# Kernel optimization log

Measured on AMD Instinct MI355X. Metric: run time of the kernel, lower is better.

Reference implementation:

```python
import jax, jax.numpy as jnp
import numpy as np

N, D = 8192, 4096


def setup_inputs() -> dict:
    key = jax.random.key(0)
    k1, k2, k3 = jax.random.split(key, 3)
    x = jax.random.normal(k1, (N, D), jnp.float32)
    W = jax.random.normal(k2, (D, D), jnp.float32) / np.sqrt(D)  # nn.Linear weight [out,in]
    b = jax.random.normal(k3, (D,), jnp.float32) * 0.01
    recency_weight = jnp.full((1,), -0.1, jnp.float32)
    return {"x": x, "W": W, "b": b, "recency_weight": recency_weight}


def reference(x, W, b, recency_weight):
    # linear -> relu projection
    x_proj = jax.nn.relu(x @ W.T + b)  # [N, D]
    # self-similarity
    scores = x_proj @ x_proj.T  # [N, N]
    n = scores.shape[0]
    idx = jnp.arange(n)
    # triu mask with diagonal=0 (use_current_timestep=False): keep strictly lower triangle
    mask = idx[None, :] >= idx[:, None]
    scores = jnp.where(mask, -jnp.inf, scores)
    # recency bias: toeplitz(arange(n)) == |i - j|, zeroed on masked positions
    rec = jnp.abs(idx[:, None] - idx[None, :]).astype(scores.dtype)
    rec = jnp.where(mask, 0.0, rec)
    scores = scores + recency_weight[0] * rec
    # row 0 is fully masked (-inf everywhere); replace with finite values to avoid
    # NaN in softmax -- the row is overwritten with zeros afterwards anyway.
    scores = scores.at[0].set(0.0)
    attn = jax.nn.softmax(scores, axis=1)
    attn = attn.at[0].set(0.0)  # matches scores[0] = zeros in the torch code
    return attn
```

## Files before the change

### kernel.cpp

```cpp
#include <hip/hip_runtime.h>
#include <hip/hip_bf16.h>
#include <stdint.h>

typedef _Float16 f16_t;
typedef f16_t f16x8_t __attribute__((ext_vector_type(8)));
typedef f16_t f16x4_t __attribute__((ext_vector_type(4)));
typedef float f32x4_t __attribute__((ext_vector_type(4)));

#define NROWS 8192
#define DDIM  4096
#define BK 32
#define KTILES (DDIM / BK)
#define LSTR 40

__device__ __forceinline__ void gload16(const void* g, void* s) {
  __builtin_amdgcn_global_load_lds(
      (const __attribute__((address_space(1))) void*)g,
      (__attribute__((address_space(3))) void*)s, 16, 0, 0);
}

__global__ __launch_bounds__(256) void k_split(const float* __restrict__ in,
                                               f16_t* __restrict__ hi,
                                               f16_t* __restrict__ lo) {
  const long i = ((long)blockIdx.x * 256 + threadIdx.x) * 4;
  const float4 v = *reinterpret_cast<const float4*>(in + i);
  float vv[4] = {v.x, v.y, v.z, v.w};
  f16x4_t h, l;
#pragma unroll
  for (int c = 0; c < 4; ++c) {
    f16_t hh = (f16_t)vv[c];
    h[c] = hh;
    l[c] = (f16_t)(vv[c] - (float)hh);
  }
  *reinterpret_cast<f16x4_t*>(hi + i) = h;
  *reinterpret_cast<f16x4_t*>(lo + i) = l;
}

typedef f16_t lds4_t[4][256][BK];

__device__ __forceinline__ void gemm_core256_g1(
    const f16_t* __restrict__ pAh, const f16_t* __restrict__ pAl, long lda,
    const f16_t* __restrict__ pBh, const f16_t* __restrict__ pBl, long ldb,
    lds4_t* sm, f32x4_t (&acc)[8][4]) {
  const int t = threadIdx.x, lane = t & 63, w = t >> 6;
  const int fr = lane & 15, kg = lane >> 4;
  const int wr = (w >> 2) * 128, wc = (w & 3) * 64;
  const int w32 = w * 32;
  const int sr0 = w32 + (lane >> 2);
  const int sg = (((lane & 3) ^ ((lane >> 3) & 3)) * 8);
  const int kge = (kg ^ ((fr >> 1) & 3)) * 8;

#pragma unroll
  for (int m = 0; m < 8; ++m)
#pragma unroll
    for (int n = 0; n < 4; ++n) acc[m][n] = f32x4_t{0.f, 0.f, 0.f, 0.f};

  const f16_t* gAh = pAh + (long)sr0 * lda + sg;
  const f16_t* gAl = pAl + (long)sr0 * lda + sg;
  const f16_t* gBh = pBh + (long)sr0 * ldb + sg;
  const f16_t* gBl = pBl + (long)sr0 * ldb + sg;
  const long a16 = 16 * lda, b16 = 16 * ldb;

  auto issue = [&](int buf, int plane, const f16_t* g, long ld16, int k0) {
    gload16(g + k0, &sm[buf][plane][w32][0]);
    gload16(g + ld16 + k0, &sm[buf][plane][w32 + 16][0]);
  };

  f16x8_t ah[8], al[8], bh[4], bl[4];
  auto read8 = [&](f16x8_t(&R)[8], int buf, int plane) {
#pragma unroll
    for (int m = 0; m < 8; ++m)
      R[m] = *reinterpret_cast<const f16x8_t*>(&sm[buf][plane][wr + m * 16 + fr][kge]);
  };
  auto read4 = [&](f16x8_t(&R)[4], int buf, int plane) {
#pragma unroll
    for (int n = 0; n < 4; ++n)
      R[n] = *reinterpret_cast<const f16x8_t*>(&sm[buf][plane][wc + n * 16 + fr][kge]);
  };
  auto mfma32 = [&](f16x8_t(&A)[8], f16x8_t(&B)[4]) {
    __builtin_amdgcn_s_setprio(1);
#pragma unroll
    for (int m = 0; m < 8; ++m)
#pragma unroll
      for (int n = 0; n < 4; ++n)
        acc[m][n] = __builtin_amdgcn_mfma_f32_16x16x32_f16(A[m], B[n], acc[m][n], 0, 0, 0);
    __builtin_amdgcn_s_setprio(0);
  };

  issue(0, 0, gAh, a16, 0);
  issue(0, 2, gBh, b16, 0);
  issue(0, 3, gBl, b16, 0);
  issue(0, 1, gAl, a16, 0);
  asm volatile("s_waitcnt vmcnt(0)" ::: "memory");
  __builtin_amdgcn_s_barrier();

  for (int kt = 0; kt < KTILES - 1; ++kt) {
    const int c = kt & 1;
    const int k0 = (kt + 1) * BK;
    issue(c ^ 1, 0, gAh, a16, k0);
    issue(c ^ 1, 2, gBh, b16, k0);
    issue(c ^ 1, 3, gBl, b16, k0);
    read8(ah, c, 0);
    read4(bh, c, 2);
    read4(bl, c, 3);
    asm volatile("s_waitcnt lgkmcnt(0)" ::: "memory");
    mfma32(ah, bh);
    mfma32(ah, bl);
    asm volatile("s_waitcnt vmcnt(6)" ::: "memory");
    __builtin_amdgcn_s_barrier();
    read8(al, c, 1);
    issue(c ^ 1, 1, gAl, a16, k0);
    asm volatile("s_waitcnt lgkmcnt(0)" ::: "memory");
    mfma32(al, bh);
    asm volatile("s_waitcnt vmcnt(2)" ::: "memory");
    __builtin_amdgcn_s_barrier();
  }
  {
    const int c = (KTILES - 1) & 1;
    read8(ah, c, 0);
    read4(bh, c, 2);
    read4(bl, c, 3);
    asm volatile("s_waitcnt lgkmcnt(0)" ::: "memory");
    mfma32(ah, bh);
    mfma32(ah, bl);
    asm volatile("s_waitcnt vmcnt(0)" ::: "memory");
    __builtin_amdgcn_s_barrier();
    read8(al, c, 1);
    asm volatile("s_waitcnt lgkmcnt(0)" ::: "memory");
    mfma32(al, bh);
  }
}

typedef f16_t lds3_t[3][256][BK];

__device__ __forceinline__ void gemm_core256_g2(
    const f16_t* __restrict__ pAh, long lda,
    const f16_t* __restrict__ pBh, const f16_t* __restrict__ pBl, long ldb,
    lds3_t* sm, f32x4_t (&acc)[8][4], bool diag) {
  const int t = threadIdx.x, lane = t & 63, w = t >> 6;
  const int fr = lane & 15, kg = lane >> 4;
  const int wr = (w >> 2) * 128, wc = (w & 3) * 64;
  const int w32 = w * 32;
  const int sr0 = w32 + (lane >> 2);
  const int sg = (((lane & 3) ^ ((lane >> 3) & 3)) * 8);
  const int kge = (kg ^ ((fr >> 1) & 3)) * 8;
  const bool skipw = diag && (wr == 0) && (wc >= 128);

#pragma unroll
  for (int m = 0; m < 8; ++m)
#pragma unroll
    for (int n = 0; n < 4; ++n) acc[m][n] = f32x4_t{0.f, 0.f, 0.f, 0.f};

  const f16_t* gAh = pAh + (long)sr0 * lda + sg;
  const f16_t* gBh = pBh + (long)sr0 * ldb + sg;
  const f16_t* gBl = pBl + (long)sr0 * ldb + sg;
  const long a16 = 16 * lda, b16 = 16 * ldb;

  auto issue = [&](int buf, int plane, const f16_t* g, long ld16, int k0) {
    gload16(g + k0, &sm[buf][plane][w32][0]);
    gload16(g + ld16 + k0, &sm[buf][plane][w32 + 16][0]);
  };

  f16x8_t ah[8], bh[4], bl[4];
  auto read8 = [&](f16x8_t(&R)[8], int buf, int plane) {
#pragma unroll
    for (int m = 0; m < 8; ++m)
      R[m] = *reinterpret_cast<const f16x8_t*>(&sm[buf][plane][wr + m * 16 + fr][kge]);
  };
  auto read4 = [&](f16x8_t(&R)[4], int buf, int plane) {
#pragma unroll
    for (int n = 0; n < 4; ++n)
      R[n] = *reinterpret_cast<const f16x8_t*>(&sm[buf][plane][wc + n * 16 + fr][kge]);
  };
  auto mfma32 = [&](f16x8_t(&A)[8], f16x8_t(&B)[4]) {
    __builtin_amdgcn_s_setprio(1);
#pragma unroll
    for (int m = 0; m < 8; ++m)
#pragma unroll
      for (int n = 0; n < 4; ++n)
        acc[m][n] = __builtin_amdgcn_mfma_f32_16x16x32_f16(A[m], B[n], acc[m][n], 0, 0, 0);
    __builtin_amdgcn_s_setprio(0);
  };

  issue(0, 0, gAh, a16, 0);
  issue(0, 1, gBh, b16, 0);
  issue(0, 2, gBl, b16, 0);
  asm volatile("s_waitcnt vmcnt(0)" ::: "memory");
  __builtin_amdgcn_s_barrier();

  for (int kt = 0; kt < KTILES - 1; ++kt) {
    const int c = kt & 1;
    const int k0 = (kt + 1) * BK;
    issue(c ^ 1, 0, gAh, a16, k0);
    issue(c ^ 1, 1, gBh, b16, k0);
    if (!skipw) {
      read8(ah, c, 0);
      read4(bh, c, 1);
      asm volatile("s_waitcnt lgkmcnt(0)" ::: "memory");
      mfma32(ah, bh);
    }
    asm volatile("s_waitcnt vmcnt(4)" ::: "memory");
    __builtin_amdgcn_s_barrier();
    if (!skipw) {
      read4(bl, c, 2);
    }
    issue(c ^ 1, 2, gBl, b16, k0);
    if (!skipw) {
      asm volatile("s_waitcnt lgkmcnt(0)" ::: "memory");
      mfma32(ah, bl);
    }
    asm volatile("s_waitcnt vmcnt(2)" ::: "memory");
    __builtin_amdgcn_s_barrier();
  }
  {
    const int c = (KTILES - 1) & 1;
    if (!skipw) {
      read8(ah, c, 0);
      read4(bh, c, 1);
      asm volatile("s_waitcnt lgkmcnt(0)" ::: "memory");
      mfma32(ah, bh);
    }
    asm volatile("s_waitcnt vmcnt(0)" ::: "memory");
    __builtin_amdgcn_s_barrier();
    if (!skipw) {
      read4(bl, c, 2);
      asm volatile("s_waitcnt lgkmcnt(0)" ::: "memory");
      mfma32(ah, bl);
    }
  }
}

__global__ __launch_bounds__(512, 2) void k_gemm1_256(
    const f16_t* __restrict__ xh, const f16_t* __restrict__ xl,
    const f16_t* __restrict__ Wh, const f16_t* __restrict__ Wl,
    const float* __restrict__ bias,
    f16_t* __restrict__ xph, f16_t* __restrict__ xpl) {
  extern __shared__ char smraw[];
  lds4_t* sm = (lds4_t*)smraw;

  int bid = (int)blockIdx.x;
  bid = (bid & 7) * 64 + (bid >> 3);
  const int bx = bid & 15, by = bid >> 4;
  const long brow = (long)by * 256, bcol = (long)bx * 256;

  f32x4_t acc[8][4];
  gemm_core256_g1(xh + brow * DDIM, xl + brow * DDIM, DDIM,
                  Wh + bcol * DDIM, Wl + bcol * DDIM, DDIM, sm, acc);

  const int t = threadIdx.x, lane = t & 63, w = t >> 6;
  const int wr = (w >> 2) * 128, wc = (w & 3) * 64;
  const int cr = (lane >> 4) * 4, cc = lane & 15;
#pragma unroll
  for (int n = 0; n < 4; ++n) {
    const long col = bcol + wc + n * 16 + cc;
    const float bb = bias[col];
#pragma unroll
    for (int m = 0; m < 8; ++m) {
      const long row0 = brow + wr + m * 16 + cr;
#pragma unroll
      for (int r = 0; r < 4; ++r) {
        const float v = fmaxf(acc[m][n][r] + bb, 0.f);
        const f16_t h = (f16_t)v;
        xph[(row0 + r) * (long)DDIM + col] = h;
        xpl[(row0 + r) * (long)DDIM + col] = (f16_t)(v - (float)h);
      }
    }
  }
}

__global__ __launch_bounds__(512, 2) void k_gemm2_256(
    const f16_t* __restrict__ xph, const f16_t* __restrict__ xpl,
    const float* __restrict__ rwp, float* __restrict__ out) {
  extern __shared__ char smraw[];
  lds3_t* sm = (lds3_t*)smraw;

  int bid = (int)blockIdx.x;
  bid = (bid & 7) * 66 + (bid >> 3);
  int by = (int)((sqrtf(8.f * (float)bid + 1.f) - 1.f) * 0.5f);
  while ((by + 1) * (by + 2) / 2 <= bid) ++by;
  while (by * (by + 1) / 2 > bid) --by;
  const int bx = bid - by * (by + 1) / 2;

  const long brow = (long)by * 256, bcol = (long)bx * 256;
  f32x4_t acc[8][4];
  gemm_core256_g2(xph + brow * DDIM, DDIM,
                  xph + bcol * DDIM, xpl + bcol * DDIM, DDIM, sm, acc, bx == by);

  const float rw = rwp[0];
  const int t = threadIdx.x, lane = t & 63, w = t >> 6;
  const int wr = (w >> 2) * 128, wc = (w & 3) * 64;
  const int cr = (lane >> 4) * 4, cc = lane & 15;
#pragma unroll
  for (int n = 0; n < 4; ++n) {
    const long gj = bcol + wc + n * 16 + cc;
#pragma unroll
    for (int m = 0; m < 8; ++m) {
      const long gi0 = brow + wr + m * 16 + cr;
#pragma unroll
      for (int r = 0; r < 4; ++r) {
        const long gi = gi0 + r;
        out[gi * (long)NROWS + gj] = acc[m][n][r] + rw * (float)(gi - gj);
      }
    }
  }
}

__device__ __forceinline__ void stage_split(const float* __restrict__ src, long ld,
                                            f16_t (&hi)[128][LSTR],
                                            f16_t (&lo)[128][LSTR],
                                            int t) {
#pragma unroll
  for (int i = 0; i < 4; ++i) {
    const int f = i * 256 + t;
    const int row = f >> 3;
    const int kq = (f & 7) << 2;
    const float4 v = *reinterpret_cast<const float4*>(src + (long)row * ld + kq);
    float vv[4] = {v.x, v.y, v.z, v.w};
    f16x4_t h, l;
#pragma unroll
    for (int c = 0; c < 4; ++c) {
      f16_t hh = (f16_t)vv[c];
      h[c] = hh;
      l[c] = (f16_t)(vv[c] - (float)hh);
    }
    *reinterpret_cast<f16x4_t*>(&hi[row][kq]) = h;
    *reinterpret_cast<f16x4_t*>(&lo[row][kq]) = l;
  }
}

__global__ __launch_bounds__(256) void k_gemm1_slow(
    const float* __restrict__ x, const float* __restrict__ W,
    const float* __restrict__ bias,
    f16_t* __restrict__ xph, f16_t* __restrict__ xpl) {
  __shared__ alignas(16) f16_t Ahi[128][LSTR];
  __shared__ alignas(16) f16_t Alo[128][LSTR];
  __shared__ alignas(16) f16_t Bhi[128][LSTR];
  __shared__ alignas(16) f16_t Blo[128][LSTR];

  const long brow = (long)blockIdx.y * 128;
  const long bcol = (long)blockIdx.x * 128;
  const int t = threadIdx.x, lane = t & 63;
  const int wr = ((t >> 6) >> 1) * 64, wc = ((t >> 6) & 1) * 64;
  const int fr = lane & 15, kg = lane >> 4;

  f32x4_t acc[4][4];
#pragma unroll
  for (int m = 0; m < 4; ++m)
#pragma unroll
    for (int n = 0; n < 4; ++n) acc[m][n] = f32x4_t{0.f, 0.f, 0.f, 0.f};

  const float* Abase = x + brow * DDIM;
  const float* Bbase = W + bcol * DDIM;
  for (int k0 = 0; k0 < DDIM; k0 += BK) {
    __syncthreads();
    stage_split(Abase + k0, DDIM, Ahi, Alo, t);
    stage_split(Bbase + k0, DDIM, Bhi, Blo, t);
    __syncthreads();

    f16x8_t ah[4], al[4], bh[4], bl[4];
#pragma unroll
    for (int m = 0; m < 4; ++m) {
      ah[m] = *reinterpret_cast<const f16x8_t*>(&Ahi[wr + m * 16 + fr][kg * 8]);
      al[m] = *reinterpret_cast<const f16x8_t*>(&Alo[wr + m * 16 + fr][kg * 8]);
      bh[m] = *reinterpret_cast<const f16x8_t*>(&Bhi[wc + m * 16 + fr][kg * 8]);
      bl[m] = *reinterpret_cast<const f16x8_t*>(&Blo[wc + m * 16 + fr][kg * 8]);
    }
#pragma unroll
    for (int m = 0; m < 4; ++m)
#pragma unroll
      for (int n = 0; n < 4; ++n) {
        acc[m][n] = __builtin_amdgcn_mfma_f32_16x16x32_f16(ah[m], bh[n], acc[m][n], 0, 0, 0);
        acc[m][n] = __builtin_amdgcn_mfma_f32_16x16x32_f16(ah[m], bl[n], acc[m][n], 0, 0, 0);
        acc[m][n] = __builtin_amdgcn_mfma_f32_16x16x32_f16(al[m], bh[n], acc[m][n], 0, 0, 0);
      }
  }

  const int cr = (lane >> 4) * 4, cc = lane & 15;
#pragma unroll
  for (int n = 0; n < 4; ++n) {
    const long col = bcol + wc + n * 16 + cc;
    const float bb = bias[col];
#pragma unroll
    for (int m = 0; m < 4; ++m) {
      const long row0 = brow + wr + m * 16 + cr;
#pragma unroll
      for (int r = 0; r < 4; ++r) {
        const float v = fmaxf(acc[m][n][r] + bb, 0.f);
        const f16_t h = (f16_t)v;
        xph[(row0 + r) * (long)DDIM + col] = h;
        xpl[(row0 + r) * (long)DDIM + col] = (f16_t)(v - (float)h);
      }
    }
  }
}

__global__ __launch_bounds__(256) void k_row_softmax(float* __restrict__ out, int n) {
  const int i = blockIdx.x;
  float* row = out + (size_t)i * n;
  const int L = i;
  const int t = threadIdx.x;
  __shared__ float redm[4], reds[4];

  float m = -3.0e38f, s = 0.f;
  for (int j = t; j < L; j += 256) {
    const float v = row[j];
    const float M = fmaxf(m, v);
    s = s * __expf(m - M) + __expf(v - M);
    m = M;
  }
#pragma unroll
  for (int o = 32; o > 0; o >>= 1) {
    const float om = __shfl_down(m, o, 64);
    const float os = __shfl_down(s, o, 64);
    const float M = fmaxf(m, om);
    s = s * __expf(m - M) + os * __expf(om - M);
    m = M;
  }
  if ((t & 63) == 0) { redm[t >> 6] = m; reds[t >> 6] = s; }
  __syncthreads();
  const float M4 = fmaxf(fmaxf(redm[0], redm[1]), fmaxf(redm[2], redm[3]));
  const float S4 = reds[0] * __expf(redm[0] - M4) + reds[1] * __expf(redm[1] - M4) +
                   reds[2] * __expf(redm[2] - M4) + reds[3] * __expf(redm[3] - M4);
  const float inv = (L > 0) ? 1.f / S4 : 0.f;

  for (int j = t; j < n; j += 256) {
    row[j] = (j < L) ? __expf(row[j] - M4) * inv : 0.f;
  }
}

extern "C" void kernel_launch(void* const* d_in, const int* in_sizes, int n_in,
                              void* d_out, int out_size, void* d_ws, size_t ws_size,
                              hipStream_t stream) {
  (void)in_sizes; (void)n_in; (void)out_size;
  const float* x = (const float*)d_in[0];
  const float* W = (const float*)d_in[1];
  const float* b = (const float*)d_in[2];
  const float* rw = (const float*)d_in[3];
  float* out = (float*)d_out;

  const size_t NX = (size_t)NROWS * DDIM;
  const size_t NW = (size_t)DDIM * DDIM;
  char* ws = (char*)d_ws;
  f16_t* xph = (f16_t*)ws;
  f16_t* xpl = (f16_t*)(ws + NX * 2);

  const int LDSB1 = 2 * 4 * 256 * BK * 2;
  const int LDSB2 = 2 * 3 * 256 * BK * 2;
  (void)hipFuncSetAttribute(reinterpret_cast<const void*>(k_gemm1_256),
                            hipFuncAttributeMaxDynamicSharedMemorySize, LDSB1);
  (void)hipFuncSetAttribute(reinterpret_cast<const void*>(k_gemm2_256),
                            hipFuncAttributeMaxDynamicSharedMemorySize, LDSB2);

  const size_t need_full = NX * 4  + NX * 4  + NW * 4 ;
  if (ws_size >= need_full) {
    f16_t* xh = (f16_t*)(ws + NX * 4);
    f16_t* xl = (f16_t*)(ws + NX * 6);
    f16_t* Wh = (f16_t*)(ws + NX * 8);
    f16_t* Wl = (f16_t*)(ws + NX * 8 + NW * 2);
    k_split<<<(int)(NX / 1024), 256, 0, stream>>>(x, xh, xl);
    k_split<<<(int)(NW / 1024), 256, 0, stream>>>(W, Wh, Wl);
    k_gemm1_256<<<512, 512, LDSB1, stream>>>(xh, xl, Wh, Wl, b, xph, xpl);
  } else {
    k_gemm1_slow<<<dim3(DDIM / 128, NROWS / 128), 256, 0, stream>>>(x, W, b, xph, xpl);
  }

  const int ntri = (NROWS / 256) * (NROWS / 256 + 1) / 2;
  k_gemm2_256<<<ntri, 512, LDSB2, stream>>>(xph, xpl, rw, out);
  k_row_softmax<<<NROWS, 256, 0, stream>>>(out, NROWS);
}
```

Before: 1.422 ms.

## Pack diagonal tiles two per block and drop explicit LDS waits before MFMA

The second GEMM grid goes from 528 triangular tiles to exactly 512 blocks. The first 16 blocks each process two half-work diagonal tiles in sequence, and the remaining 496 blocks each take one strictly-lower off-diagonal tile through a new index mapping. With two blocks per CU this is meant to fit the launch into a single wave and remove the small tail of leftover blocks. Separately, the explicit lgkmcnt(0) waits before the MFMA groups are removed in both GEMM cores, leaving the compiler to insert the finer-grained waits it needs so LDS reads can overlap with math. The risk is that the compiler's waits turn out no better than before, and the paired diagonal blocks become a longer critical path.

Result: faster. 1.387 ms (-2.5%).

```diff
diff --git a/kernel.cpp b/kernel.cpp
--- a/kernel.cpp
+++ b/kernel.cpp
@@ -103,14 +103,12 @@
     read8(ah, c, 0);
     read4(bh, c, 2);
     read4(bl, c, 3);
-    asm volatile("s_waitcnt lgkmcnt(0)" ::: "memory");
     mfma32(ah, bh);
     mfma32(ah, bl);
     asm volatile("s_waitcnt vmcnt(6)" ::: "memory");
     __builtin_amdgcn_s_barrier();
     read8(al, c, 1);
     issue(c ^ 1, 1, gAl, a16, k0);
-    asm volatile("s_waitcnt lgkmcnt(0)" ::: "memory");
     mfma32(al, bh);
     asm volatile("s_waitcnt vmcnt(2)" ::: "memory");
     __builtin_amdgcn_s_barrier();
@@ -120,13 +118,11 @@
     read8(ah, c, 0);
     read4(bh, c, 2);
     read4(bl, c, 3);
-    asm volatile("s_waitcnt lgkmcnt(0)" ::: "memory");
     mfma32(ah, bh);
     mfma32(ah, bl);
     asm volatile("s_waitcnt vmcnt(0)" ::: "memory");
     __builtin_amdgcn_s_barrier();
     read8(al, c, 1);
-    asm volatile("s_waitcnt lgkmcnt(0)" ::: "memory");
     mfma32(al, bh);
   }
 }
@@ -196,7 +192,6 @@
     if (!skipw) {
       read8(ah, c, 0);
       read4(bh, c, 1);
-      asm volatile("s_waitcnt lgkmcnt(0)" ::: "memory");
       mfma32(ah, bh);
     }
     asm volatile("s_waitcnt vmcnt(4)" ::: "memory");
@@ -206,7 +201,6 @@
     }
     issue(c ^ 1, 2, gBl, b16, k0);
     if (!skipw) {
-      asm volatile("s_waitcnt lgkmcnt(0)" ::: "memory");
       mfma32(ah, bl);
     }
     asm volatile("s_waitcnt vmcnt(2)" ::: "memory");
@@ -217,14 +211,12 @@
     if (!skipw) {
       read8(ah, c, 0);
       read4(bh, c, 1);
-      asm volatile("s_waitcnt lgkmcnt(0)" ::: "memory");
       mfma32(ah, bh);
     }
     asm volatile("s_waitcnt vmcnt(0)" ::: "memory");
     __builtin_amdgcn_s_barrier();
     if (!skipw) {
       read4(bl, c, 2);
-      asm volatile("s_waitcnt lgkmcnt(0)" ::: "memory");
       mfma32(ah, bl);
     }
   }
@@ -268,40 +260,56 @@
   }
 }
 
+__device__ __forceinline__ void g2_epilogue(f32x4_t (&acc)[8][4], long brow, long bcol,
+                                            float rw, float* __restrict__ out) {
+  const int t = threadIdx.x, lane = t & 63, w = t >> 6;
+  const int wr = (w >> 2) * 128, wc = (w & 3) * 64;
+  const int cr = (lane >> 4) * 4, cc = lane & 15;
+#pragma unroll
+  for (int n = 0; n < 4; ++n) {
+    const long gj = bcol + wc + n * 16 + cc;
+#pragma unroll
+    for (int m = 0; m < 8; ++m) {
+      const long gi0 = brow + wr + m * 16 + cr;
+#pragma unroll
+      for (int r = 0; r < 4; ++r) {
+        const long gi = gi0 + r;
+        out[gi * (long)NROWS + gj] = acc[m][n][r] + rw * (float)(gi - gj);
+      }
+    }
+  }
+}
+
 __global__ __launch_bounds__(512, 2) void k_gemm2_256(
     const f16_t* __restrict__ xph, const f16_t* __restrict__ xpl,
     const float* __restrict__ rwp, float* __restrict__ out) {
   extern __shared__ char smraw[];
   lds3_t* sm = (lds3_t*)smraw;
-
-  int bid = (int)blockIdx.x;
-  bid = (bid & 7) * 66 + (bid >> 3);
-  int by = (int)((sqrtf(8.f * (float)bid + 1.f) - 1.f) * 0.5f);
-  while ((by + 1) * (by + 2) / 2 <= bid) ++by;
-  while (by * (by + 1) / 2 > bid) --by;
-  const int bx = bid - by * (by + 1) / 2;
-
-  const long brow = (long)by * 256, bcol = (long)bx * 256;
+  const float rw = rwp[0];
+  const int bid = (int)blockIdx.x;
+
   f32x4_t acc[8][4];
-  gemm_core256_g2(xph + brow * DDIM, DDIM,
-                  xph + bcol * DDIM, xpl + bcol * DDIM, DDIM, sm, acc, bx == by);
-
-  const float rw = rwp[0];
-  const int t = threadIdx.x, lane = t & 63, w = t >> 6;
-  const int wr = (w >> 2) * 128, wc = (w & 3) * 64;
-  const int cr = (lane >> 4) * 4, cc = lane & 15;
-#pragma unroll
-  for (int n = 0; n < 4; ++n) {
-    const long gj = bcol + wc + n * 16 + cc;
-#pragma unroll
-    for (int m = 0; m < 8; ++m) {
-      const long gi0 = brow + wr + m * 16 + cr;
-#pragma unroll
-      for (int r = 0; r < 4; ++r) {
-        const long gi = gi0 + r;
-        out[gi * (long)NROWS + gj] = acc[m][n][r] + rw * (float)(gi - gj);
-      }
-    }
+  if (bid < 16) {
+#pragma unroll 1
+    for (int d = 0; d < 2; ++d) {
+      const int by = bid * 2 + d;
+      const long brow = (long)by * 256, bcol = brow;
+      gemm_core256_g2(xph + brow * DDIM, DDIM,
+                      xph + bcol * DDIM, xpl + bcol * DDIM, DDIM, sm, acc, true);
+      g2_epilogue(acc, brow, bcol, rw, out);
+      __syncthreads();
+    }
+  } else {
+    int p = bid - 16;
+    p = (p & 7) * 62 + (p >> 3);
+    int by = (int)((1.f + sqrtf(1.f + 8.f * (float)p)) * 0.5f);
+    while (by * (by + 1) / 2 <= p) ++by;
+    while (by * (by - 1) / 2 > p) --by;
+    const int bx = p - by * (by - 1) / 2;
+    const long brow = (long)by * 256, bcol = (long)bx * 256;
+    gemm_core256_g2(xph + brow * DDIM, DDIM,
+                    xph + bcol * DDIM, xpl + bcol * DDIM, DDIM, sm, acc, false);
+    g2_epilogue(acc, brow, bcol, rw, out);
   }
 }
 
@@ -464,7 +472,6 @@
     k_gemm1_slow<<<dim3(DDIM / 128, NROWS / 128), 256, 0, stream>>>(x, W, b, xph, xpl);
   }
 
-  const int ntri = (NROWS / 256) * (NROWS / 256 + 1) / 2;
-  k_gemm2_256<<<ntri, 512, LDSB2, stream>>>(xph, xpl, rw, out);
+  k_gemm2_256<<<512, 512, LDSB2, stream>>>(xph, xpl, rw, out);
   k_row_softmax<<<NROWS, 256, 0, stream>>>(out, NROWS);
 }
```

## Retile second GEMM to 128x256 triangular tiles with higher occupancy

Applied to the files above, without the earlier changes.

Replaces the 256x256 triangular-tile self-similarity GEMM with a 128x256 tile kernel that uses a single packed LDS buffer and smaller accumulators, allowing four blocks per CU. The finer row granularity cuts wasted work on diagonal tiles and rebalances the triangular grid. It also removes the explicit lgkmcnt waits before the MFMAs in the first GEMM, leaving LDS read ordering to the compiler. The trade-off is less operand reuse per tile and more global traffic, plus a risk that the compiler's implicit waits will not cover the removed ones.

New measurement: 1.734 ms. +22.0%, slower.

```diff
diff --git a/kernel.cpp b/kernel.cpp
--- a/kernel.cpp
+++ b/kernel.cpp
@@ -103,14 +103,12 @@
     read8(ah, c, 0);
     read4(bh, c, 2);
     read4(bl, c, 3);
-    asm volatile("s_waitcnt lgkmcnt(0)" ::: "memory");
     mfma32(ah, bh);
     mfma32(ah, bl);
     asm volatile("s_waitcnt vmcnt(6)" ::: "memory");
     __builtin_amdgcn_s_barrier();
     read8(al, c, 1);
     issue(c ^ 1, 1, gAl, a16, k0);
-    asm volatile("s_waitcnt lgkmcnt(0)" ::: "memory");
     mfma32(al, bh);
     asm volatile("s_waitcnt vmcnt(2)" ::: "memory");
     __builtin_amdgcn_s_barrier();
@@ -120,113 +118,12 @@
     read8(ah, c, 0);
     read4(bh, c, 2);
     read4(bl, c, 3);
-    asm volatile("s_waitcnt lgkmcnt(0)" ::: "memory");
     mfma32(ah, bh);
     mfma32(ah, bl);
     asm volatile("s_waitcnt vmcnt(0)" ::: "memory");
     __builtin_amdgcn_s_barrier();
     read8(al, c, 1);
-    asm volatile("s_waitcnt lgkmcnt(0)" ::: "memory");
     mfma32(al, bh);
-  }
-}
-
-typedef f16_t lds3_t[3][256][BK];
-
-__device__ __forceinline__ void gemm_core256_g2(
-    const f16_t* __restrict__ pAh, long lda,
-    const f16_t* __restrict__ pBh, const f16_t* __restrict__ pBl, long ldb,
-    lds3_t* sm, f32x4_t (&acc)[8][4], bool diag) {
-  const int t = threadIdx.x, lane = t & 63, w = t >> 6;
-  const int fr = lane & 15, kg = lane >> 4;
-  const int wr = (w >> 2) * 128, wc = (w & 3) * 64;
-  const int w32 = w * 32;
-  const int sr0 = w32 + (lane >> 2);
-  const int sg = (((lane & 3) ^ ((lane >> 3) & 3)) * 8);
-  const int kge = (kg ^ ((fr >> 1) & 3)) * 8;
-  const bool skipw = diag && (wr == 0) && (wc >= 128);
-
-#pragma unroll
-  for (int m = 0; m < 8; ++m)
-#pragma unroll
-    for (int n = 0; n < 4; ++n) acc[m][n] = f32x4_t{0.f, 0.f, 0.f, 0.f};
-
-  const f16_t* gAh = pAh + (long)sr0 * lda + sg;
-  const f16_t* gBh = pBh + (long)sr0 * ldb + sg;
-  const f16_t* gBl = pBl + (long)sr0 * ldb + sg;
-  const long a16 = 16 * lda, b16 = 16 * ldb;
-
-  auto issue = [&](int buf, int plane, const f16_t* g, long ld16, int k0) {
-    gload16(g + k0, &sm[buf][plane][w32][0]);
-    gload16(g + ld16 + k0, &sm[buf][plane][w32 + 16][0]);
-  };
-
-  f16x8_t ah[8], bh[4], bl[4];
-  auto read8 = [&](f16x8_t(&R)[8], int buf, int plane) {
-#pragma unroll
-    for (int m = 0; m < 8; ++m)
-      R[m] = *reinterpret_cast<const f16x8_t*>(&sm[buf][plane][wr + m * 16 + fr][kge]);
-  };
-  auto read4 = [&](f16x8_t(&R)[4], int buf, int plane) {
-#pragma unroll
-    for (int n = 0; n < 4; ++n)
-      R[n] = *reinterpret_cast<const f16x8_t*>(&sm[buf][plane][wc + n * 16 + fr][kge]);
-  };
-  auto mfma32 = [&](f16x8_t(&A)[8], f16x8_t(&B)[4]) {
-    __builtin_amdgcn_s_setprio(1);
-#pragma unroll
-    for (int m = 0; m < 8; ++m)
-#pragma unroll
-      for (int n = 0; n < 4; ++n)
-        acc[m][n] = __builtin_amdgcn_mfma_f32_16x16x32_f16(A[m], B[n], acc[m][n], 0, 0, 0);
-    __builtin_amdgcn_s_setprio(0);
-  };
-
-  issue(0, 0, gAh, a16, 0);
-  issue(0, 1, gBh, b16, 0);
-  issue(0, 2, gBl, b16, 0);
-  asm volatile("s_waitcnt vmcnt(0)" ::: "memory");
-  __builtin_amdgcn_s_barrier();
-
-  for (int kt = 0; kt < KTILES - 1; ++kt) {
-    const int c = kt & 1;
-    const int k0 = (kt + 1) * BK;
-    issue(c ^ 1, 0, gAh, a16, k0);
-    issue(c ^ 1, 1, gBh, b16, k0);
-    if (!skipw) {
-      read8(ah, c, 0);
-      read4(bh, c, 1);
-      asm volatile("s_waitcnt lgkmcnt(0)" ::: "memory");
-      mfma32(ah, bh);
-    }
-    asm volatile("s_waitcnt vmcnt(4)" ::: "memory");
-    __builtin_amdgcn_s_barrier();
-    if (!skipw) {
-      read4(bl, c, 2);
-    }
-    issue(c ^ 1, 2, gBl, b16, k0);
-    if (!skipw) {
-      asm volatile("s_waitcnt lgkmcnt(0)" ::: "memory");
-      mfma32(ah, bl);
-    }
-    asm volatile("s_waitcnt vmcnt(2)" ::: "memory");
-    __builtin_amdgcn_s_barrier();
-  }
-  {
-    const int c = (KTILES - 1) & 1;
-    if (!skipw) {
-      read8(ah, c, 0);
-      read4(bh, c, 1);
-      asm volatile("s_waitcnt lgkmcnt(0)" ::: "memory");
-      mfma32(ah, bh);
-    }
-    asm volatile("s_waitcnt vmcnt(0)" ::: "memory");
-    __builtin_amdgcn_s_barrier();
-    if (!skipw) {
-      read4(bl, c, 2);
-      asm volatile("s_waitcnt lgkmcnt(0)" ::: "memory");
-      mfma32(ah, bl);
-    }
   }
 }
 
@@ -268,33 +165,117 @@
   }
 }
 
-__global__ __launch_bounds__(512, 2) void k_gemm2_256(
+#define G2_ROWS 640
+typedef f16_t ldsg2_t[G2_ROWS][BK];
+
+__global__ __launch_bounds__(512, 4) void k_gemm2_128(
     const f16_t* __restrict__ xph, const f16_t* __restrict__ xpl,
     const float* __restrict__ rwp, float* __restrict__ out) {
   extern __shared__ char smraw[];
-  lds3_t* sm = (lds3_t*)smraw;
-
-  int bid = (int)blockIdx.x;
-  bid = (bid & 7) * 66 + (bid >> 3);
-  int by = (int)((sqrtf(8.f * (float)bid + 1.f) - 1.f) * 0.5f);
-  while ((by + 1) * (by + 2) / 2 <= bid) ++by;
-  while (by * (by + 1) / 2 > bid) --by;
-  const int bx = bid - by * (by + 1) / 2;
-
-  const long brow = (long)by * 256, bcol = (long)bx * 256;
-  f32x4_t acc[8][4];
-  gemm_core256_g2(xph + brow * DDIM, DDIM,
-                  xph + bcol * DDIM, xpl + bcol * DDIM, DDIM, sm, acc, bx == by);
+  ldsg2_t* sm = (ldsg2_t*)smraw;
+
+  int p = (int)blockIdx.x;
+  p = (p & 7) * 132 + (p >> 3);
+  auto ftri = [](int y) { return (((y + 1) >> 1)) * ((y >> 1) + 1); };
+  int by = (int)(2.f * sqrtf((float)p));
+  if (by > 63) by = 63;
+  while (by > 0 && ftri(by) > p) --by;
+  while (ftri(by + 1) <= p) ++by;
+  const int bx = p - ftri(by);
+
+  const long brow = (long)by * 128, bcol = (long)bx * 256;
+  const f16_t* __restrict__ pA  = xph + brow * DDIM;
+  const f16_t* __restrict__ pBh = xph + bcol * DDIM;
+  const f16_t* __restrict__ pBl = xpl + bcol * DDIM;
+
+  const int t = threadIdx.x, lane = t & 63, w = t >> 6;
+  const int fr = lane & 15, kg = lane >> 4;
+  const int wr = (w >> 2) * 64, wc = (w & 3) * 64;
+  const int w16 = w * 16, w32 = w * 32;
+  const int lrow = lane >> 2;
+  const int sg = (((lane & 3) ^ ((lane >> 3) & 3)) * 8);
+  const int kge = (kg ^ ((fr >> 1) & 3)) * 8;
+
+  f32x4_t acc[4][4];
+#pragma unroll
+  for (int m = 0; m < 4; ++m)
+#pragma unroll
+    for (int n = 0; n < 4; ++n) acc[m][n] = f32x4_t{0.f, 0.f, 0.f, 0.f};
+
+  const f16_t* gA  = pA + (long)(w16 + lrow) * DDIM + sg;
+  const f16_t* gBh = pBh + (long)(w32 + lrow) * DDIM + sg;
+  const f16_t* gBl = pBl + (long)(w32 + lrow) * DDIM + sg;
+  const long ld16 = 16 * (long)DDIM;
+
+  auto issueP0 = [&](int buf, int k0) {
+    gload16(gA + k0, &sm[buf][w16][0]);
+    gload16(gBh + k0, &sm[buf][128 + w32][0]);
+    gload16(gBh + ld16 + k0, &sm[buf][128 + w32 + 16][0]);
+  };
+  auto issueP1 = [&](int buf, int k0) {
+    gload16(gBl + k0, &sm[buf][384 + w32][0]);
+    gload16(gBl + ld16 + k0, &sm[buf][384 + w32 + 16][0]);
+  };
+
+  f16x8_t ah[4], bh[4], bl[4];
+  auto readA = [&](int buf) {
+#pragma unroll
+    for (int m = 0; m < 4; ++m)
+      ah[m] = *reinterpret_cast<const f16x8_t*>(&sm[buf][wr + m * 16 + fr][kge]);
+  };
+  auto readB = [&](f16x8_t(&R)[4], int buf, int base) {
+#pragma unroll
+    for (int n = 0; n < 4; ++n)
+      R[n] = *reinterpret_cast<const f16x8_t*>(&sm[buf][base + wc + n * 16 + fr][kge]);
+  };
+  auto mfma16 = [&](f16x8_t(&A)[4], f16x8_t(&B)[4]) {
+    __builtin_amdgcn_s_setprio(1);
+#pragma unroll
+    for (int m = 0; m < 4; ++m)
+#pragma unroll
+      for (int n = 0; n < 4; ++n)
+        acc[m][n] = __builtin_amdgcn_mfma_f32_16x16x32_f16(A[m], B[n], acc[m][n], 0, 0, 0);
+    __builtin_amdgcn_s_setprio(0);
+  };
+
+  issueP0(0, 0);
+  issueP1(0, 0);
+  asm volatile("s_waitcnt vmcnt(0)" ::: "memory");
+  __builtin_amdgcn_s_barrier();
+
+  for (int kt = 0; kt < KTILES - 1; ++kt) {
+    const int c = kt & 1;
+    const int k0 = (kt + 1) * BK;
+    issueP0(c ^ 1, k0);
+    readA(c);
+    readB(bh, c, 128);
+    mfma16(ah, bh);
+    asm volatile("s_waitcnt vmcnt(3)" ::: "memory");
+    __builtin_amdgcn_s_barrier();
+    readB(bl, c, 384);
+    issueP1(c ^ 1, k0);
+    mfma16(ah, bl);
+    asm volatile("s_waitcnt vmcnt(2)" ::: "memory");
+    __builtin_amdgcn_s_barrier();
+  }
+  {
+    const int c = (KTILES - 1) & 1;
+    readA(c);
+    readB(bh, c, 128);
+    mfma16(ah, bh);
+    asm volatile("s_waitcnt vmcnt(0)" ::: "memory");
+    __builtin_amdgcn_s_barrier();
+    readB(bl, c, 384);
+    mfma16(ah, bl);
+  }
 
   const float rw = rwp[0];
-  const int t = threadIdx.x, lane = t & 63, w = t >> 6;
-  const int wr = (w >> 2) * 128, wc = (w & 3) * 64;
   const int cr = (lane >> 4) * 4, cc = lane & 15;
 #pragma unroll
   for (int n = 0; n < 4; ++n) {
     const long gj = bcol + wc + n * 16 + cc;
 #pragma unroll
-    for (int m = 0; m < 8; ++m) {
+    for (int m = 0; m < 4; ++m) {
       const long gi0 = brow + wr + m * 16 + cr;
 #pragma unroll
       for (int r = 0; r < 4; ++r) {
@@ -445,10 +426,10 @@
   f16_t* xpl = (f16_t*)(ws + NX * 2);
 
   const int LDSB1 = 2 * 4 * 256 * BK * 2;
-  const int LDSB2 = 2 * 3 * 256 * BK * 2;
+  const int LDSB2 = 2 * G2_ROWS * BK * 2;
   (void)hipFuncSetAttribute(reinterpret_cast<const void*>(k_gemm1_256),
                             hipFuncAttributeMaxDynamicSharedMemorySize, LDSB1);
-  (void)hipFuncSetAttribute(reinterpret_cast<const void*>(k_gemm2_256),
+  (void)hipFuncSetAttribute(reinterpret_cast<const void*>(k_gemm2_128),
                             hipFuncAttributeMaxDynamicSharedMemorySize, LDSB2);
 
   const size_t need_full = NX * 4  + NX * 4  + NW * 4 ;
@@ -464,7 +445,6 @@
     k_gemm1_slow<<<dim3(DDIM / 128, NROWS / 128), 256, 0, stream>>>(x, W, b, xph, xpl);
   }
 
-  const int ntri = (NROWS / 256) * (NROWS / 256 + 1) / 2;
-  k_gemm2_256<<<ntri, 512, LDSB2, stream>>>(xph, xpl, rw, out);
+  k_gemm2_128<<<1056, 512, LDSB2, stream>>>(xph, xpl, rw, out);
   k_row_softmax<<<NROWS, 256, 0, stream>>>(out, NROWS);
 }
```

## Split-K the triangular similarity GEMM and fold partial sums into softmax

Applied to the files above, without the earlier changes.

The second GEMM now splits its K dimension in half, launching twice as many blocks over the 528 lower-triangular tiles. The upper K half writes its partial tile to a workspace buffer, which reuses the region freed after the first GEMM. The row softmax adds those partials back while reading scores. This is meant to reduce the tail-wave imbalance of 528 tiles on the available block slots. It also drops the explicit lgkmcnt waits and the diagonal-tile warp skip, and in exchange adds extra global traffic for writing and re-reading the partial tiles.

After: 1.385 ms. -2.6%, faster.

```diff
diff --git a/kernel.cpp b/kernel.cpp
--- a/kernel.cpp
+++ b/kernel.cpp
@@ -103,14 +103,12 @@
     read8(ah, c, 0);
     read4(bh, c, 2);
     read4(bl, c, 3);
-    asm volatile("s_waitcnt lgkmcnt(0)" ::: "memory");
     mfma32(ah, bh);
     mfma32(ah, bl);
     asm volatile("s_waitcnt vmcnt(6)" ::: "memory");
     __builtin_amdgcn_s_barrier();
     read8(al, c, 1);
     issue(c ^ 1, 1, gAl, a16, k0);
-    asm volatile("s_waitcnt lgkmcnt(0)" ::: "memory");
     mfma32(al, bh);
     asm volatile("s_waitcnt vmcnt(2)" ::: "memory");
     __builtin_amdgcn_s_barrier();
@@ -120,14 +118,50 @@
     read8(ah, c, 0);
     read4(bh, c, 2);
     read4(bl, c, 3);
-    asm volatile("s_waitcnt lgkmcnt(0)" ::: "memory");
     mfma32(ah, bh);
     mfma32(ah, bl);
     asm volatile("s_waitcnt vmcnt(0)" ::: "memory");
     __builtin_amdgcn_s_barrier();
     read8(al, c, 1);
-    asm volatile("s_waitcnt lgkmcnt(0)" ::: "memory");
     mfma32(al, bh);
+  }
+}
+
+__global__ __launch_bounds__(512, 2) void k_gemm1_256(
+    const f16_t* __restrict__ xh, const f16_t* __restrict__ xl,
+    const f16_t* __restrict__ Wh, const f16_t* __restrict__ Wl,
+    const float* __restrict__ bias,
+    f16_t* __restrict__ xph, f16_t* __restrict__ xpl) {
+  extern __shared__ char smraw[];
+  lds4_t* sm = (lds4_t*)smraw;
+
+  int bid = (int)blockIdx.x;
+  bid = (bid & 7) * 64 + (bid >> 3);
+  const int bx = bid & 15, by = bid >> 4;
+  const long brow = (long)by * 256, bcol = (long)bx * 256;
+
+  f32x4_t acc[8][4];
+  gemm_core256_g1(xh + brow * DDIM, xl + brow * DDIM, DDIM,
+                  Wh + bcol * DDIM, Wl + bcol * DDIM, DDIM, sm, acc);
+
+  const int t = threadIdx.x, lane = t & 63, w = t >> 6;
+  const int wr = (w >> 2) * 128, wc = (w & 3) * 64;
+  const int cr = (lane >> 4) * 4, cc = lane & 15;
+#pragma unroll
+  for (int n = 0; n < 4; ++n) {
+    const long col = bcol + wc + n * 16 + cc;
+    const float bb = bias[col];
+#pragma unroll
+    for (int m = 0; m < 8; ++m) {
+      const long row0 = brow + wr + m * 16 + cr;
+#pragma unroll
+      for (int r = 0; r < 4; ++r) {
+        const float v = fmaxf(acc[m][n][r] + bb, 0.f);
+        const f16_t h = (f16_t)v;
+        xph[(row0 + r) * (long)DDIM + col] = h;
+        xpl[(row0 + r) * (long)DDIM + col] = (f16_t)(v - (float)h);
+      }
+    }
   }
 }
 
@@ -136,7 +170,7 @@
 __device__ __forceinline__ void gemm_core256_g2(
     const f16_t* __restrict__ pAh, long lda,
     const f16_t* __restrict__ pBh, const f16_t* __restrict__ pBl, long ldb,
-    lds3_t* sm, f32x4_t (&acc)[8][4], bool diag) {
+    lds3_t* sm, f32x4_t (&acc)[8][4], int kt0, int ktn) {
   const int t = threadIdx.x, lane = t & 63, w = t >> 6;
   const int fr = lane & 15, kg = lane >> 4;
   const int wr = (w >> 2) * 128, wc = (w & 3) * 64;
@@ -144,7 +178,6 @@
   const int sr0 = w32 + (lane >> 2);
   const int sg = (((lane & 3) ^ ((lane >> 3) & 3)) * 8);
   const int kge = (kg ^ ((fr >> 1) & 3)) * 8;
-  const bool skipw = diag && (wr == 0) && (wc >= 128);
 
 #pragma unroll
   for (int m = 0; m < 8; ++m)
@@ -182,124 +215,102 @@
     __builtin_amdgcn_s_setprio(0);
   };
 
-  issue(0, 0, gAh, a16, 0);
-  issue(0, 1, gBh, b16, 0);
-  issue(0, 2, gBl, b16, 0);
+  const int kb = kt0 * BK;
+  issue(0, 0, gAh, a16, kb);
+  issue(0, 1, gBh, b16, kb);
+  issue(0, 2, gBl, b16, kb);
   asm volatile("s_waitcnt vmcnt(0)" ::: "memory");
   __builtin_amdgcn_s_barrier();
 
-  for (int kt = 0; kt < KTILES - 1; ++kt) {
-    const int c = kt & 1;
-    const int k0 = (kt + 1) * BK;
+  for (int it = 0; it < ktn - 1; ++it) {
+    const int c = it & 1;
+    const int k0 = (kt0 + it + 1) * BK;
     issue(c ^ 1, 0, gAh, a16, k0);
     issue(c ^ 1, 1, gBh, b16, k0);
-    if (!skipw) {
-      read8(ah, c, 0);
-      read4(bh, c, 1);
-      asm volatile("s_waitcnt lgkmcnt(0)" ::: "memory");
-      mfma32(ah, bh);
-    }
+    read8(ah, c, 0);
+    read4(bh, c, 1);
+    mfma32(ah, bh);
     asm volatile("s_waitcnt vmcnt(4)" ::: "memory");
     __builtin_amdgcn_s_barrier();
-    if (!skipw) {
-      read4(bl, c, 2);
-    }
+    read4(bl, c, 2);
     issue(c ^ 1, 2, gBl, b16, k0);
-    if (!skipw) {
-      asm volatile("s_waitcnt lgkmcnt(0)" ::: "memory");
-      mfma32(ah, bl);
-    }
+    mfma32(ah, bl);
     asm volatile("s_waitcnt vmcnt(2)" ::: "memory");
     __builtin_amdgcn_s_barrier();
   }
   {
-    const int c = (KTILES - 1) & 1;
-    if (!skipw) {
-      read8(ah, c, 0);
-      read4(bh, c, 1);
-      asm volatile("s_waitcnt lgkmcnt(0)" ::: "memory");
-      mfma32(ah, bh);
-    }
+    const int c = (ktn - 1) & 1;
+    read8(ah, c, 0);
+    read4(bh, c, 1);
+    mfma32(ah, bh);
     asm volatile("s_waitcnt vmcnt(0)" ::: "memory");
     __builtin_amdgcn_s_barrier();
-    if (!skipw) {
-      read4(bl, c, 2);
-      asm volatile("s_waitcnt lgkmcnt(0)" ::: "memory");
-      mfma32(ah, bl);
-    }
-  }
-}
-
-__global__ __launch_bounds__(512, 2) void k_gemm1_256(
-    const f16_t* __restrict__ xh, const f16_t* __restrict__ xl,
-    const f16_t* __restrict__ Wh, const f16_t* __restrict__ Wl,
-    const float* __restrict__ bias,
-    f16_t* __restrict__ xph, f16_t* __restrict__ xpl) {
+    read4(bl, c, 2);
+    mfma32(ah, bl);
+  }
+}
+
+template <bool SPLITK>
+__global__ __launch_bounds__(512, 2) void k_gemm2(
+    const f16_t* __restrict__ xph, const f16_t* __restrict__ xpl,
+    const float* __restrict__ rwp, float* __restrict__ out,
+    float* __restrict__ part) {
   extern __shared__ char smraw[];
-  lds4_t* sm = (lds4_t*)smraw;
-
-  int bid = (int)blockIdx.x;
-  bid = (bid & 7) * 64 + (bid >> 3);
-  const int bx = bid & 15, by = bid >> 4;
+  lds3_t* sm = (lds3_t*)smraw;
+
+  int id = (int)blockIdx.x;
+  int tidx, khalf;
+  if (SPLITK) {
+    id = (id & 7) * 132 + (id >> 3);
+    khalf = (id >= 528) ? 1 : 0;
+    tidx = id - khalf * 528;
+  } else {
+    id = (id & 7) * 66 + (id >> 3);
+    khalf = 0;
+    tidx = id;
+  }
+  int by = (int)((sqrtf(8.f * (float)tidx + 1.f) - 1.f) * 0.5f);
+  while ((by + 1) * (by + 2) / 2 <= tidx) ++by;
+  while (by * (by + 1) / 2 > tidx) --by;
+  const int bx = tidx - by * (by + 1) / 2;
+
   const long brow = (long)by * 256, bcol = (long)bx * 256;
-
   f32x4_t acc[8][4];
-  gemm_core256_g1(xh + brow * DDIM, xl + brow * DDIM, DDIM,
-                  Wh + bcol * DDIM, Wl + bcol * DDIM, DDIM, sm, acc);
+  gemm_core256_g2(xph + brow * DDIM, DDIM,
+                  xph + bcol * DDIM, xpl + bcol * DDIM, DDIM, sm, acc,
+                  SPLITK ? khalf * (KTILES / 2) : 0, SPLITK ? (KTILES / 2) : KTILES);
 
   const int t = threadIdx.x, lane = t & 63, w = t >> 6;
   const int wr = (w >> 2) * 128, wc = (w & 3) * 64;
   const int cr = (lane >> 4) * 4, cc = lane & 15;
-#pragma unroll
-  for (int n = 0; n < 4; ++n) {
-    const long col = bcol + wc + n * 16 + cc;
-    const float bb = bias[col];
-#pragma unroll
-    for (int m = 0; m < 8; ++m) {
-      const long row0 = brow + wr + m * 16 + cr;
-#pragma unroll
-      for (int r = 0; r < 4; ++r) {
-        const float v = fmaxf(acc[m][n][r] + bb, 0.f);
-        const f16_t h = (f16_t)v;
-        xph[(row0 + r) * (long)DDIM + col] = h;
-        xpl[(row0 + r) * (long)DDIM + col] = (f16_t)(v - (float)h);
+
+  if (!SPLITK || khalf == 0) {
+    const float rw = rwp[0];
+#pragma unroll
+    for (int n = 0; n < 4; ++n) {
+      const long gj = bcol + wc + n * 16 + cc;
+#pragma unroll
+      for (int m = 0; m < 8; ++m) {
+        const long gi0 = brow + wr + m * 16 + cr;
+#pragma unroll
+        for (int r = 0; r < 4; ++r) {
+          const long gi = gi0 + r;
+          out[gi * (long)NROWS + gj] = acc[m][n][r] + rw * (float)(gi - gj);
+        }
       }
     }
-  }
-}
-
-__global__ __launch_bounds__(512, 2) void k_gemm2_256(
-    const f16_t* __restrict__ xph, const f16_t* __restrict__ xpl,
-    const float* __restrict__ rwp, float* __restrict__ out) {
-  extern __shared__ char smraw[];
-  lds3_t* sm = (lds3_t*)smraw;
-
-  int bid = (int)blockIdx.x;
-  bid = (bid & 7) * 66 + (bid >> 3);
-  int by = (int)((sqrtf(8.f * (float)bid + 1.f) - 1.f) * 0.5f);
-  while ((by + 1) * (by + 2) / 2 <= bid) ++by;
-  while (by * (by + 1) / 2 > bid) --by;
-  const int bx = bid - by * (by + 1) / 2;
-
-  const long brow = (long)by * 256, bcol = (long)bx * 256;
-  f32x4_t acc[8][4];
-  gemm_core256_g2(xph + brow * DDIM, DDIM,
-                  xph + bcol * DDIM, xpl + bcol * DDIM, DDIM, sm, acc, bx == by);
-
-  const float rw = rwp[0];
-  const int t = threadIdx.x, lane = t & 63, w = t >> 6;
-  const int wr = (w >> 2) * 128, wc = (w & 3) * 64;
-  const int cr = (lane >> 4) * 4, cc = lane & 15;
-#pragma unroll
-  for (int n = 0; n < 4; ++n) {
-    const long gj = bcol + wc + n * 16 + cc;
-#pragma unroll
-    for (int m = 0; m < 8; ++m) {
-      const long gi0 = brow + wr + m * 16 + cr;
-#pragma unroll
-      for (int r = 0; r < 4; ++r) {
-        const long gi = gi0 + r;
-        out[gi * (long)NROWS + gj] = acc[m][n][r] + rw * (float)(gi - gj);
+  } else {
+    float* pt = part + (size_t)tidx * 65536;
+#pragma unroll
+    for (int n = 0; n < 4; ++n) {
+      const int lj = wc + n * 16 + cc;
+#pragma unroll
+      for (int m = 0; m < 8; ++m) {
+        const int li0 = wr + m * 16 + cr;
+#pragma unroll
+        for (int r = 0; r < 4; ++r) {
+          pt[(li0 + r) * 256 + lj] = acc[m][n][r];
+        }
       }
     }
   }
@@ -394,16 +405,28 @@
   }
 }
 
-__global__ __launch_bounds__(256) void k_row_softmax(float* __restrict__ out, int n) {
+__global__ __launch_bounds__(256) void k_row_softmax(float* __restrict__ out,
+                                                     const float* __restrict__ part,
+                                                     int n) {
   const int i = blockIdx.x;
   float* row = out + (size_t)i * n;
   const int L = i;
   const int t = threadIdx.x;
   __shared__ float redm[4], reds[4];
 
+  const int rt = i >> 8;
+  const float* prow =
+      part ? (part + ((size_t)(rt * (rt + 1) / 2) << 16) + ((size_t)(i & 255) << 8)) : nullptr;
+
+  auto val = [&](int j) -> float {
+    float v = row[j];
+    if (part) v += prow[((size_t)(j >> 8) << 16) + (j & 255)];
+    return v;
+  };
+
   float m = -3.0e38f, s = 0.f;
   for (int j = t; j < L; j += 256) {
-    const float v = row[j];
+    const float v = val(j);
     const float M = fmaxf(m, v);
     s = s * __expf(m - M) + __expf(v - M);
     m = M;
@@ -424,7 +447,7 @@
   const float inv = (L > 0) ? 1.f / S4 : 0.f;
 
   for (int j = t; j < n; j += 256) {
-    row[j] = (j < L) ? __expf(row[j] - M4) * inv : 0.f;
+    row[j] = (j < L) ? __expf(val(j) - M4) * inv : 0.f;
   }
 }
 
@@ -448,7 +471,9 @@
   const int LDSB2 = 2 * 3 * 256 * BK * 2;
   (void)hipFuncSetAttribute(reinterpret_cast<const void*>(k_gemm1_256),
                             hipFuncAttributeMaxDynamicSharedMemorySize, LDSB1);
-  (void)hipFuncSetAttribute(reinterpret_cast<const void*>(k_gemm2_256),
+  (void)hipFuncSetAttribute(reinterpret_cast<const void*>(&k_gemm2<true>),
+                            hipFuncAttributeMaxDynamicSharedMemorySize, LDSB2);
+  (void)hipFuncSetAttribute(reinterpret_cast<const void*>(&k_gemm2<false>),
                             hipFuncAttributeMaxDynamicSharedMemorySize, LDSB2);
 
   const size_t need_full = NX * 4  + NX * 4  + NW * 4 ;
@@ -457,14 +482,15 @@
     f16_t* xl = (f16_t*)(ws + NX * 6);
     f16_t* Wh = (f16_t*)(ws + NX * 8);
     f16_t* Wl = (f16_t*)(ws + NX * 8 + NW * 2);
+    float* part = (float*)(ws + NX * 4);
     k_split<<<(int)(NX / 1024), 256, 0, stream>>>(x, xh, xl);
     k_split<<<(int)(NW / 1024), 256, 0, stream>>>(W, Wh, Wl);
     k_gemm1_256<<<512, 512, LDSB1, stream>>>(xh, xl, Wh, Wl, b, xph, xpl);
+    k_gemm2<true><<<1056, 512, LDSB2, stream>>>(xph, xpl, rw, out, part);
+    k_row_softmax<<<NROWS, 256, 0, stream>>>(out, part, NROWS);
   } else {
     k_gemm1_slow<<<dim3(DDIM / 128, NROWS / 128), 256, 0, stream>>>(x, W, b, xph, xpl);
-  }
-
-  const int ntri = (NROWS / 256) * (NROWS / 256 + 1) / 2;
-  k_gemm2_256<<<ntri, 512, LDSB2, stream>>>(xph, xpl, rw, out);
-  k_row_softmax<<<NROWS, 256, 0, stream>>>(out, NROWS);
-}
+    k_gemm2<false><<<528, 512, LDSB2, stream>>>(xph, xpl, rw, out, nullptr);
+    k_row_softmax<<<NROWS, 256, 0, stream>>>(out, nullptr, NROWS);
+  }
+}
```
